# Kernel optimization log

Measured on AMD Instinct MI355X. Metric: run time of the kernel, lower is better.

The kernel has to match this reference:

```python
import jax, jax.numpy as jnp
import numpy as np

WINDOW_SIZES = (1, 2, 3)
COV_DIM = 128
MEM_DIM = 128
BATCH = 8192


def setup_inputs() -> dict:
    rng = np.random.default_rng(0)
    sizes = rng.integers(16, 64, size=BATCH)
    total = int(sizes.sum())  # ~327k tokens
    key = jax.random.key(0)
    ks = jax.random.split(key, 10)
    s = 0.05
    inp = {
        "x": jax.random.normal(ks[0], (total, COV_DIM), jnp.float32),
        "sizes": jnp.asarray(sizes, jnp.int32),
    }
    for i, w in enumerate(WINDOW_SIZES):
        inp[f"conv_w{i}"] = jax.random.normal(ks[1 + 2 * i], (MEM_DIM, COV_DIM, w), jnp.float32) * s
        inp[f"conv_b{i}"] = jax.random.normal(ks[2 + 2 * i], (MEM_DIM,), jnp.float32) * s
    inp["lin_w"] = jax.random.normal(ks[7], (MEM_DIM, len(WINDOW_SIZES) * MEM_DIM), jnp.float32) * s
    inp["lin_b"] = jax.random.normal(ks[8], (MEM_DIM,), jnp.float32) * s
    return inp


def _temporal_conv(x, w, b):
    # x: [T, C], w: [M, C, k] -> [T-k+1, M]  (valid 1D conv, as nn.Conv1d)
    y = jax.lax.conv_general_dilated(
        x.T[None],  # [1, C, T]
        w,
        window_strides=(1,),
        padding="VALID",
        dimension_numbers=("NCH", "OIH", "NCH"),
    )[0]  # [M, L]
    return y.T + b


def _dmax(h, sizes, window_size, batch):
    # Ragged per-segment max over dim 0 of the concatenated conv output.
    # Segment i covers rows [off_i, off_i + sizes[i] - window_size + 1) where
    # off_i is the exclusive cumsum of sizes (DMax advances start_idx by sizes[i]).
    L = h.shape[0]  # total - window_size + 1
    cum = jnp.cumsum(sizes)  # [B], inclusive
    p = jnp.arange(L)
    seg = jnp.searchsorted(cum, p, side="right")  # segment owning row p
    valid = p + (window_size - 1) < cum[seg]  # within sizes[i]-w+1 prefix
    seg = jnp.where(valid, seg, batch)  # dump invalid rows in a trash segment
    return jax.ops.segment_max(h, seg, num_segments=batch + 1)[:batch]


def reference(x, sizes, conv_w0, conv_b0, conv_w1, conv_b1, conv_w2, conv_b2, lin_w, lin_b):
    batch = sizes.shape[0]
    convs = ((conv_w0, conv_b0), (conv_w1, conv_b1), (conv_w2, conv_b2))
    pools = []
    for wsz, (cw, cb) in zip(WINDOW_SIZES, convs):
        h = jax.nn.relu(_temporal_conv(x, cw, cb))  # [T-w+1, M]
        pools.append(_dmax(h, sizes, wsz, batch))  # [B, M]
    concat = jnp.concatenate(pools, axis=1)  # [B, 3M]
    return jnp.tanh(concat @ lin_w.T + lin_b)  # [B, M]
```

## Files before the change

kernel.cpp:

```cpp
#include <hip/hip_runtime.h>
#include <hip/hip_bf16.h>

typedef __bf16 bf16x8 __attribute__((ext_vector_type(8)));
typedef __bf16 bf16x4 __attribute__((ext_vector_type(4)));
typedef float  f32x4  __attribute__((ext_vector_type(4)));

#define MFMA16(a, b, c) __builtin_amdgcn_mfma_f32_16x16x32_bf16((a), (b), (c), 0, 0, 0)

__global__ void k_prep(const int* __restrict__ sizes, int* __restrict__ offsets,
                       const float* __restrict__ w0, const float* __restrict__ w1,
                       const float* __restrict__ w2, const float* __restrict__ lw,
                       __bf16* __restrict__ Wpack,
                       __bf16* __restrict__ Lhi, __bf16* __restrict__ Llo) {
  const int bid = blockIdx.x, t = threadIdx.x;
  if (bid == 240) {
    __shared__ int part[256];
    const int base = t * 32;
    int v[32];
    int s = 0;
#pragma unroll
    for (int i = 0; i < 32; ++i) { v[i] = sizes[base + i]; s += v[i]; }
    part[t] = s;
    __syncthreads();
    for (int d = 1; d < 256; d <<= 1) {
      int add = (t >= d) ? part[t - d] : 0;
      __syncthreads();
      part[t] += add;
      __syncthreads();
    }
    int run = (t == 0) ? 0 : part[t - 1];
#pragma unroll
    for (int i = 0; i < 32; ++i) { offsets[base + i] = run; run += v[i]; }
  } else if (bid < 48) {
    const int nt = bid, sl = nt >> 3, f = nt & 7;
    const int kt = t >> 6, lane = t & 63;
    const float* src; int kw, jj;
    if      (sl == 0) { src = w0; kw = 1; jj = 0; }
    else if (sl == 1) { src = w1; kw = 2; jj = 0; }
    else if (sl == 2) { src = w1; kw = 2; jj = 1; }
    else if (sl == 3) { src = w2; kw = 3; jj = 0; }
    else if (sl == 4) { src = w2; kw = 3; jj = 1; }
    else              { src = w2; kw = 3; jj = 2; }
    const int feat  = f * 16 + (lane & 15);
    const int cbase = kt * 32 + ((lane >> 4) << 3);
    __bf16* dst = Wpack + ((((nt * 4 + kt) << 6) + lane) << 3);
#pragma unroll
    for (int j = 0; j < 8; ++j)
      dst[j] = (__bf16)src[(feat * 128 + cbase + j) * kw + jj];
  } else {
    const int idx = (bid - 48) * 256 + t;
    const int j = idx & 7, lane = (idx >> 3) & 63, rest = idx >> 9;
    const int kt = rest % 12, nt = rest / 12;
    const int o = nt * 16 + (lane & 15);
    const int q = kt * 32 + ((lane >> 4) << 3) + j;
    const float v = lw[o * 384 + q];
    const __bf16 hi = (__bf16)v;
    Lhi[idx] = hi;
    Llo[idx] = (__bf16)(v - (float)hi);
  }
}

__global__ __launch_bounds__(256, 3)
void k_conv(const float* __restrict__ x, const int* __restrict__ sizes,
            const int* __restrict__ offsets,
            const float* __restrict__ cb0, const float* __restrict__ cb1,
            const float* __restrict__ cb2,
            const bf16x8* __restrict__ Wpack,
            __bf16* __restrict__ Phi, __bf16* __restrict__ Plo) {
  __shared__ __bf16 xh[64 * 136];
  const int b = blockIdx.x;
  const int s = sizes[b];
  const long off = offsets[b];
  const int t = threadIdx.x;
  const int MT = (s + 15) >> 4;

  const int quads = s << 5;
  for (int qi = t; qi < quads; qi += 256) {
    const int e = qi << 2, r = e >> 7, c = e & 127;
    const float4 v = *(const float4*)(x + (off + r) * 128 + c);
    bf16x4 h; h[0] = (__bf16)v.x; h[1] = (__bf16)v.y;
              h[2] = (__bf16)v.z; h[3] = (__bf16)v.w;
    *(bf16x4*)&xh[r * 136 + c] = h;
  }
  const int padquads = ((MT << 4) - s) << 5;
  for (int qi = t; qi < padquads; qi += 256) {
    const int e = (qi << 2) + (s << 7), r = e >> 7, c = e & 127;
    *(bf16x4*)&xh[r * 136 + c] = bf16x4{(__bf16)0.f, (__bf16)0.f, (__bf16)0.f, (__bf16)0.f};
  }
  __syncthreads();

  const int wid = t >> 6, lane = t & 63;
  const int lo16 = lane & 15, g = lane >> 4;

#pragma unroll
  for (int fi = 0; fi < 2; ++fi) {
    const int ft = wid + (fi << 2);
    const int feat = ft * 16 + lo16;
    f32x4 acc[4][6];
#pragma unroll
    for (int mt = 0; mt < 4; ++mt)
#pragma unroll
      for (int sl = 0; sl < 6; ++sl)
        acc[mt][sl] = f32x4{0.f, 0.f, 0.f, 0.f};

#pragma unroll
    for (int kt = 0; kt < 4; ++kt) {
      bf16x8 bf[6];
#pragma unroll
      for (int sl = 0; sl < 6; ++sl)
        bf[sl] = Wpack[(((sl * 8 + ft) * 4 + kt) << 6) + lane];
#pragma unroll
      for (int mt = 0; mt < 4; ++mt) {
        if (mt < MT) {
          const bf16x8 a =
              *(const bf16x8*)&xh[(mt * 16 + lo16) * 136 + kt * 32 + (g << 3)];
#pragma unroll
          for (int sl = 0; sl < 6; ++sl)
            acc[mt][sl] = MFMA16(a, bf[sl], acc[mt][sl]);
        }
      }
    }

    float m1 = -1e30f, m2 = -1e30f, m3 = -1e30f;
#pragma unroll
    for (int mt = 0; mt < 4; ++mt) {
      if (mt >= MT) continue;
#pragma unroll
      for (int v = 0; v < 4; ++v) {
        float s2v;
        if (v < 3) {
          s2v = acc[mt][2][v + 1];
        } else {
          const float up = __shfl(acc[mt][2][0], lane + 16);
          const float dn = __shfl(acc[(mt < 3) ? mt + 1 : mt][2][0], lo16);
          s2v = (g < 3) ? up : dn;
        }
        float s4v;
        if (v < 3) {
          s4v = acc[mt][4][v + 1];
        } else {
          const float up = __shfl(acc[mt][4][0], lane + 16);
          const float dn = __shfl(acc[(mt < 3) ? mt + 1 : mt][4][0], lo16);
          s4v = (g < 3) ? up : dn;
        }
        float s5v;
        if (v < 2) {
          s5v = acc[mt][5][v + 2];
        } else {
          const float up = __shfl(acc[mt][5][v - 2], lane + 16);
          const float dn = __shfl(acc[(mt < 3) ? mt + 1 : mt][5][v - 2], lo16);
          s5v = (g < 3) ? up : dn;
        }
        const int lrow = mt * 16 + g * 4 + v;
        if (lrow < s)     m1 = fmaxf(m1, acc[mt][0][v]);
        if (lrow < s - 1) m2 = fmaxf(m2, acc[mt][1][v] + s2v);
        if (lrow < s - 2) m3 = fmaxf(m3, acc[mt][3][v] + s4v + s5v);
      }
    }
    m1 = fmaxf(m1, __shfl_xor(m1, 16)); m1 = fmaxf(m1, __shfl_xor(m1, 32));
    m2 = fmaxf(m2, __shfl_xor(m2, 16)); m2 = fmaxf(m2, __shfl_xor(m2, 32));
    m3 = fmaxf(m3, __shfl_xor(m3, 16)); m3 = fmaxf(m3, __shfl_xor(m3, 32));
    if (g == 0) {
      const float p1 = fmaxf(m1 + cb0[feat], 0.f);
      const float p2 = fmaxf(m2 + cb1[feat], 0.f);
      const float p3 = fmaxf(m3 + cb2[feat], 0.f);
      const __bf16 h1 = (__bf16)p1, h2 = (__bf16)p2, h3 = (__bf16)p3;
      Phi[(long)b * 384 + feat]       = h1;
      Plo[(long)b * 384 + feat]       = (__bf16)(p1 - (float)h1);
      Phi[(long)b * 384 + 128 + feat] = h2;
      Plo[(long)b * 384 + 128 + feat] = (__bf16)(p2 - (float)h2);
      Phi[(long)b * 384 + 256 + feat] = h3;
      Plo[(long)b * 384 + 256 + feat] = (__bf16)(p3 - (float)h3);
    }
  }
}

__global__ __launch_bounds__(256, 4)
void k_lin(const __bf16* __restrict__ Phi, const __bf16* __restrict__ Plo,
           const bf16x8* __restrict__ Lhi, const bf16x8* __restrict__ Llo,
           const float* __restrict__ lb, float* __restrict__ out) {
  __shared__ __bf16 ph[16 * 392];
  __shared__ __bf16 pl[16 * 392];
  const int blk = blockIdx.x, t = threadIdx.x;
  const long rbase = (long)blk * 16;
#pragma unroll
  for (int i = 0; i < 3; ++i) {
    const int ci = t + (i << 8);
    const int r = ci / 48, cc = ci % 48;
    *(int4*)&ph[r * 392 + (cc << 3)] = *(const int4*)&Phi[(rbase + r) * 384 + (cc << 3)];
    *(int4*)&pl[r * 392 + (cc << 3)] = *(const int4*)&Plo[(rbase + r) * 384 + (cc << 3)];
  }
  __syncthreads();
  const int wid = t >> 6, lane = t & 63;
  const int lo16 = lane & 15, g = lane >> 4;
#pragma unroll
  for (int ni = 0; ni < 2; ++ni) {
    const int nt = wid + (ni << 2);
    f32x4 acc = f32x4{0.f, 0.f, 0.f, 0.f};
#pragma unroll
    for (int kt = 0; kt < 12; ++kt) {
      const bf16x8 bh = Lhi[((nt * 12 + kt) << 6) + lane];
      const bf16x8 bl = Llo[((nt * 12 + kt) << 6) + lane];
      const int aoff = lo16 * 392 + kt * 32 + (g << 3);
      const bf16x8 ah = *(const bf16x8*)&ph[aoff];
      const bf16x8 al = *(const bf16x8*)&pl[aoff];
      acc = MFMA16(ah, bh, acc);
      acc = MFMA16(al, bh, acc);
      acc = MFMA16(ah, bl, acc);
    }
    const int o = nt * 16 + lo16;
    const float bias = lb[o];
#pragma unroll
    for (int v = 0; v < 4; ++v) {
      const int r = g * 4 + v;
      const float val = acc[v] + bias;
      out[(rbase + r) * 128 + o] = 1.f - 2.f / (__expf(2.f * val) + 1.f);
    }
  }
}

extern "C" void kernel_launch(void* const* d_in, const int* in_sizes, int n_in,
                              void* d_out, int out_size, void* d_ws, size_t ws_size,
                              hipStream_t stream) {
  const float* x   = (const float*)d_in[0];
  const int* sizes = (const int*)d_in[1];
  const float* w0  = (const float*)d_in[2];
  const float* cb0 = (const float*)d_in[3];
  const float* w1  = (const float*)d_in[4];
  const float* cb1 = (const float*)d_in[5];
  const float* w2  = (const float*)d_in[6];
  const float* cb2 = (const float*)d_in[7];
  const float* lw  = (const float*)d_in[8];
  const float* lb  = (const float*)d_in[9];

  char* ws = (char*)d_ws;
  size_t o = 0;
  int*    offsets = (int*)ws;                 o += 32768;
  __bf16* Wpack   = (__bf16*)(ws + o);        o += 196608;
  __bf16* Lhi     = (__bf16*)(ws + o);        o += 98304;
  __bf16* Llo     = (__bf16*)(ws + o);        o += 98304;
  __bf16* Phi     = (__bf16*)(ws + o);        o += 8192L * 384 * 2;
  __bf16* Plo     = (__bf16*)(ws + o);        o += 8192L * 384 * 2;

  k_prep<<<241, 256, 0, stream>>>(sizes, offsets, w0, w1, w2, lw, Wpack, Lhi, Llo);
  k_conv<<<8192, 256, 0, stream>>>(x, sizes, offsets, cb0, cb1, cb2,
                                   (const bf16x8*)Wpack, Phi, Plo);
  k_lin<<<512, 256, 0, stream>>>(Phi, Plo, (const bf16x8*)Lhi,
                                 (const bf16x8*)Llo, lb, (float*)d_out);
}
```

Baseline: 340.9 us.

## Process three segments per conv block to reuse weight fragments in registers

Each conv block now stages three segments into shared memory and loops over them, loading each weight fragment set once per block instead of once per segment. The six weight slices are split into two passes of three, which lowers accumulator register pressure while holding all four k-tiles of weights in registers. This cuts repeated global weight reads and the number of blocks, but triples LDS use per block (about 52KB), which limits occupancy. It also lengthens the serial work per block.

```diff
diff --git a/kernel.cpp b/kernel.cpp
--- a/kernel.cpp
+++ b/kernel.cpp
@@ -6,6 +6,8 @@
 typedef float  f32x4  __attribute__((ext_vector_type(4)));
 
 #define MFMA16(a, b, c) __builtin_amdgcn_mfma_f32_16x16x32_bf16((a), (b), (c), 0, 0, 0)
+
+#define SEGS_PER_BLOCK 3
 
 __global__ void k_prep(const int* __restrict__ sizes, int* __restrict__ offsets,
                        const float* __restrict__ w0, const float* __restrict__ w1,
@@ -67,110 +69,156 @@
             const float* __restrict__ cb2,
             const bf16x8* __restrict__ Wpack,
             __bf16* __restrict__ Phi, __bf16* __restrict__ Plo) {
-  __shared__ __bf16 xh[64 * 136];
-  const int b = blockIdx.x;
-  const int s = sizes[b];
-  const long off = offsets[b];
+  __shared__ __bf16 xh[SEGS_PER_BLOCK][64 * 136];
+  const int b0 = blockIdx.x * SEGS_PER_BLOCK;
+  const int segs = min(SEGS_PER_BLOCK, 8192 - b0);
   const int t = threadIdx.x;
-  const int MT = (s + 15) >> 4;
-
-  const int quads = s << 5;
-  for (int qi = t; qi < quads; qi += 256) {
-    const int e = qi << 2, r = e >> 7, c = e & 127;
-    const float4 v = *(const float4*)(x + (off + r) * 128 + c);
-    bf16x4 h; h[0] = (__bf16)v.x; h[1] = (__bf16)v.y;
-              h[2] = (__bf16)v.z; h[3] = (__bf16)v.w;
-    *(bf16x4*)&xh[r * 136 + c] = h;
-  }
-  const int padquads = ((MT << 4) - s) << 5;
-  for (int qi = t; qi < padquads; qi += 256) {
-    const int e = (qi << 2) + (s << 7), r = e >> 7, c = e & 127;
-    *(bf16x4*)&xh[r * 136 + c] = bf16x4{(__bf16)0.f, (__bf16)0.f, (__bf16)0.f, (__bf16)0.f};
+
+  int  sz[SEGS_PER_BLOCK];
+  long ofs[SEGS_PER_BLOCK];
+#pragma unroll
+  for (int g = 0; g < SEGS_PER_BLOCK; ++g) {
+    sz[g]  = (g < segs) ? sizes[b0 + g] : 0;
+    ofs[g] = (g < segs) ? (long)offsets[b0 + g] : 0;
+  }
+
+#pragma unroll
+  for (int g = 0; g < SEGS_PER_BLOCK; ++g) {
+    if (g >= segs) break;
+    const int s = sz[g];
+    const int MT = (s + 15) >> 4;
+    const long off = ofs[g];
+    __bf16* base = &xh[g][0];
+    const int quads = s << 5;
+    for (int qi = t; qi < quads; qi += 256) {
+      const int r = qi >> 5, c = (qi & 31) << 2;
+      const float4 v = *(const float4*)(x + (off + r) * 128 + c);
+      bf16x4 h; h[0] = (__bf16)v.x; h[1] = (__bf16)v.y;
+                h[2] = (__bf16)v.z; h[3] = (__bf16)v.w;
+      *(bf16x4*)&base[r * 136 + c] = h;
+    }
+    const int padquads = ((MT << 4) - s) << 5;
+    for (int qi = t; qi < padquads; qi += 256) {
+      const int e = (qi << 2) + (s << 7), r = e >> 7, c = e & 127;
+      *(bf16x4*)&base[r * 136 + c] =
+          bf16x4{(__bf16)0.f, (__bf16)0.f, (__bf16)0.f, (__bf16)0.f};
+    }
   }
   __syncthreads();
 
   const int wid = t >> 6, lane = t & 63;
-  const int lo16 = lane & 15, g = lane >> 4;
+  const int lo16 = lane & 15, g16 = lane >> 4;
 
 #pragma unroll
   for (int fi = 0; fi < 2; ++fi) {
     const int ft = wid + (fi << 2);
     const int feat = ft * 16 + lo16;
-    f32x4 acc[4][6];
-#pragma unroll
-    for (int mt = 0; mt < 4; ++mt)
-#pragma unroll
-      for (int sl = 0; sl < 6; ++sl)
-        acc[mt][sl] = f32x4{0.f, 0.f, 0.f, 0.f};
-
-#pragma unroll
-    for (int kt = 0; kt < 4; ++kt) {
-      bf16x8 bf[6];
-#pragma unroll
-      for (int sl = 0; sl < 6; ++sl)
-        bf[sl] = Wpack[(((sl * 8 + ft) * 4 + kt) << 6) + lane];
-#pragma unroll
-      for (int mt = 0; mt < 4; ++mt) {
-        if (mt < MT) {
-          const bf16x8 a =
-              *(const bf16x8*)&xh[(mt * 16 + lo16) * 136 + kt * 32 + (g << 3)];
-#pragma unroll
-          for (int sl = 0; sl < 6; ++sl)
-            acc[mt][sl] = MFMA16(a, bf[sl], acc[mt][sl]);
+#pragma unroll
+    for (int pass = 0; pass < 2; ++pass) {
+      bf16x8 bf[3][4];
+#pragma unroll
+      for (int sl = 0; sl < 3; ++sl)
+#pragma unroll
+        for (int kt = 0; kt < 4; ++kt)
+          bf[sl][kt] = Wpack[((((pass * 3 + sl) * 8 + ft) * 4 + kt) << 6) + lane];
+
+#pragma unroll
+      for (int g = 0; g < SEGS_PER_BLOCK; ++g) {
+        if (g >= segs) break;
+        const int s = sz[g];
+        const int MT = (s + 15) >> 4;
+        const __bf16* base = &xh[g][0];
+
+        f32x4 acc[4][3];
+#pragma unroll
+        for (int mt = 0; mt < 4; ++mt)
+#pragma unroll
+          for (int sl = 0; sl < 3; ++sl)
+            acc[mt][sl] = f32x4{0.f, 0.f, 0.f, 0.f};
+
+#pragma unroll
+        for (int kt = 0; kt < 4; ++kt) {
+#pragma unroll
+          for (int mt = 0; mt < 4; ++mt) {
+            if (mt < MT) {
+              const bf16x8 a =
+                  *(const bf16x8*)&base[(mt * 16 + lo16) * 136 + kt * 32 + (g16 << 3)];
+              acc[mt][0] = MFMA16(a, bf[0][kt], acc[mt][0]);
+              acc[mt][1] = MFMA16(a, bf[1][kt], acc[mt][1]);
+              acc[mt][2] = MFMA16(a, bf[2][kt], acc[mt][2]);
+            }
+          }
+        }
+
+        if (pass == 0) {
+          float m1 = -1e30f, m2 = -1e30f;
+#pragma unroll
+          for (int mt = 0; mt < 4; ++mt) {
+            if (mt >= MT) continue;
+#pragma unroll
+            for (int v = 0; v < 4; ++v) {
+              float s2v;
+              if (v < 3) {
+                s2v = acc[mt][2][v + 1];
+              } else {
+                const float up = __shfl(acc[mt][2][0], lane + 16);
+                const float dn = __shfl(acc[(mt < 3) ? mt + 1 : mt][2][0], lo16);
+                s2v = (g16 < 3) ? up : dn;
+              }
+              const int lrow = mt * 16 + g16 * 4 + v;
+              if (lrow < s)     m1 = fmaxf(m1, acc[mt][0][v]);
+              if (lrow < s - 1) m2 = fmaxf(m2, acc[mt][1][v] + s2v);
+            }
+          }
+          m1 = fmaxf(m1, __shfl_xor(m1, 16)); m1 = fmaxf(m1, __shfl_xor(m1, 32));
+          m2 = fmaxf(m2, __shfl_xor(m2, 16)); m2 = fmaxf(m2, __shfl_xor(m2, 32));
+          if (g16 == 0) {
+            const float p1 = fmaxf(m1 + cb0[feat], 0.f);
+            const float p2 = fmaxf(m2 + cb1[feat], 0.f);
+            const __bf16 h1 = (__bf16)p1, h2 = (__bf16)p2;
+            const long row = (long)(b0 + g) * 384;
+            Phi[row + feat]       = h1;
+            Plo[row + feat]       = (__bf16)(p1 - (float)h1);
+            Phi[row + 128 + feat] = h2;
+            Plo[row + 128 + feat] = (__bf16)(p2 - (float)h2);
+          }
+        } else {
+          float m3 = -1e30f;
+#pragma unroll
+          for (int mt = 0; mt < 4; ++mt) {
+            if (mt >= MT) continue;
+#pragma unroll
+            for (int v = 0; v < 4; ++v) {
+              float s4v;
+              if (v < 3) {
+                s4v = acc[mt][1][v + 1];
+              } else {
+                const float up = __shfl(acc[mt][1][0], lane + 16);
+                const float dn = __shfl(acc[(mt < 3) ? mt + 1 : mt][1][0], lo16);
+                s4v = (g16 < 3) ? up : dn;
+              }
+              float s5v;
+              if (v < 2) {
+                s5v = acc[mt][2][v + 2];
+              } else {
+                const float up = __shfl(acc[mt][2][v - 2], lane + 16);
+                const float dn = __shfl(acc[(mt < 3) ? mt + 1 : mt][2][v - 2], lo16);
+                s5v = (g16 < 3) ? up : dn;
+              }
+              const int lrow = mt * 16 + g16 * 4 + v;
+              if (lrow < s - 2) m3 = fmaxf(m3, acc[mt][0][v] + s4v + s5v);
+            }
+          }
+          m3 = fmaxf(m3, __shfl_xor(m3, 16)); m3 = fmaxf(m3, __shfl_xor(m3, 32));
+          if (g16 == 0) {
+            const float p3 = fmaxf(m3 + cb2[feat], 0.f);
+            const __bf16 h3 = (__bf16)p3;
+            const long row = (long)(b0 + g) * 384;
+            Phi[row + 256 + feat] = h3;
+            Plo[row + 256 + feat] = (__bf16)(p3 - (float)h3);
+          }
         }
       }
-    }
-
-    float m1 = -1e30f, m2 = -1e30f, m3 = -1e30f;
-#pragma unroll
-    for (int mt = 0; mt < 4; ++mt) {
-      if (mt >= MT) continue;
-#pragma unroll
-      for (int v = 0; v < 4; ++v) {
-        float s2v;
-        if (v < 3) {
-          s2v = acc[mt][2][v + 1];
-        } else {
-          const float up = __shfl(acc[mt][2][0], lane + 16);
-          const float dn = __shfl(acc[(mt < 3) ? mt + 1 : mt][2][0], lo16);
-          s2v = (g < 3) ? up : dn;
-        }
-        float s4v;
-        if (v < 3) {
-          s4v = acc[mt][4][v + 1];
-        } else {
-          const float up = __shfl(acc[mt][4][0], lane + 16);
-          const float dn = __shfl(acc[(mt < 3) ? mt + 1 : mt][4][0], lo16);
-          s4v = (g < 3) ? up : dn;
-        }
-        float s5v;
-        if (v < 2) {
-          s5v = acc[mt][5][v + 2];
-        } else {
-          const float up = __shfl(acc[mt][5][v - 2], lane + 16);
-          const float dn = __shfl(acc[(mt < 3) ? mt + 1 : mt][5][v - 2], lo16);
-          s5v = (g < 3) ? up : dn;
-        }
-        const int lrow = mt * 16 + g * 4 + v;
-        if (lrow < s)     m1 = fmaxf(m1, acc[mt][0][v]);
-        if (lrow < s - 1) m2 = fmaxf(m2, acc[mt][1][v] + s2v);
-        if (lrow < s - 2) m3 = fmaxf(m3, acc[mt][3][v] + s4v + s5v);
-      }
-    }
-    m1 = fmaxf(m1, __shfl_xor(m1, 16)); m1 = fmaxf(m1, __shfl_xor(m1, 32));
-    m2 = fmaxf(m2, __shfl_xor(m2, 16)); m2 = fmaxf(m2, __shfl_xor(m2, 32));
-    m3 = fmaxf(m3, __shfl_xor(m3, 16)); m3 = fmaxf(m3, __shfl_xor(m3, 32));
-    if (g == 0) {
-      const float p1 = fmaxf(m1 + cb0[feat], 0.f);
-      const float p2 = fmaxf(m2 + cb1[feat], 0.f);
-      const float p3 = fmaxf(m3 + cb2[feat], 0.f);
-      const __bf16 h1 = (__bf16)p1, h2 = (__bf16)p2, h3 = (__bf16)p3;
-      Phi[(long)b * 384 + feat]       = h1;
-      Plo[(long)b * 384 + feat]       = (__bf16)(p1 - (float)h1);
-      Phi[(long)b * 384 + 128 + feat] = h2;
-      Plo[(long)b * 384 + 128 + feat] = (__bf16)(p2 - (float)h2);
-      Phi[(long)b * 384 + 256 + feat] = h3;
-      Plo[(long)b * 384 + 256 + feat] = (__bf16)(p3 - (float)h3);
     }
   }
 }
@@ -242,9 +290,10 @@
   __bf16* Phi     = (__bf16*)(ws + o);        o += 8192L * 384 * 2;
   __bf16* Plo     = (__bf16*)(ws + o);        o += 8192L * 384 * 2;
 
+  const int nconv = (8192 + SEGS_PER_BLOCK - 1) / SEGS_PER_BLOCK;
   k_prep<<<241, 256, 0, stream>>>(sizes, offsets, w0, w1, w2, lw, Wpack, Lhi, Llo);
-  k_conv<<<8192, 256, 0, stream>>>(x, sizes, offsets, cb0, cb1, cb2,
-                                   (const bf16x8*)Wpack, Phi, Plo);
+  k_conv<<<nconv, 256, 0, stream>>>(x, sizes, offsets, cb0, cb1, cb2,
+                                    (const bf16x8*)Wpack, Phi, Plo);
   k_lin<<<512, 256, 0, stream>>>(Phi, Plo, (const bf16x8*)Lhi,
                                  (const bf16x8*)Llo, lb, (float*)d_out);
 }
```

After: 350.4 us. +2.8%, slower.

## Shift A rows in LDS to accumulate conv taps in MFMA, drop shuffles

Applied to the files above, without the earlier changes.

Instead of computing each conv tap into its own accumulator and combining them with cross-lane shuffles, the kernel now loads row-shifted A fragments (offset by one and two rows) from LDS. It accumulates all taps of each window into a single accumulator, cutting accumulators from six to three per tile. This lowers register pressure, so the launch bound rises to 4 blocks per CU, and the epilogue shuffles go away. The x staging loop is also restructured to issue all global loads before converting and storing, and two extra padding rows are zeroed. The cost is extra LDS reads per MFMA group and a slightly larger LDS buffer.

```diff
diff --git a/kernel.cpp b/kernel.cpp
--- a/kernel.cpp
+++ b/kernel.cpp
@@ -60,48 +60,63 @@
   }
 }
 
-__global__ __launch_bounds__(256, 3)
+__global__ __launch_bounds__(256, 4)
 void k_conv(const float* __restrict__ x, const int* __restrict__ sizes,
             const int* __restrict__ offsets,
             const float* __restrict__ cb0, const float* __restrict__ cb1,
             const float* __restrict__ cb2,
             const bf16x8* __restrict__ Wpack,
             __bf16* __restrict__ Phi, __bf16* __restrict__ Plo) {
-  __shared__ __bf16 xh[64 * 136];
+  __shared__ __bf16 xh[66 * 136];
   const int b = blockIdx.x;
   const int s = sizes[b];
   const long off = offsets[b];
   const int t = threadIdx.x;
   const int MT = (s + 15) >> 4;
 
-  const int quads = s << 5;
-  for (int qi = t; qi < quads; qi += 256) {
-    const int e = qi << 2, r = e >> 7, c = e & 127;
-    const float4 v = *(const float4*)(x + (off + r) * 128 + c);
-    bf16x4 h; h[0] = (__bf16)v.x; h[1] = (__bf16)v.y;
-              h[2] = (__bf16)v.z; h[3] = (__bf16)v.w;
-    *(bf16x4*)&xh[r * 136 + c] = h;
-  }
-  const int padquads = ((MT << 4) - s) << 5;
-  for (int qi = t; qi < padquads; qi += 256) {
-    const int e = (qi << 2) + (s << 7), r = e >> 7, c = e & 127;
-    *(bf16x4*)&xh[r * 136 + c] = bf16x4{(__bf16)0.f, (__bf16)0.f, (__bf16)0.f, (__bf16)0.f};
+  {
+    const int quads = s << 5;
+    float4 v[8];
+#pragma unroll
+    for (int i = 0; i < 8; ++i) {
+      const int qi = t + (i << 8);
+      if (qi < quads) {
+        const int r = qi >> 5, c = (qi & 31) << 2;
+        v[i] = *(const float4*)(x + (off + r) * 128 + c);
+      }
+    }
+#pragma unroll
+    for (int i = 0; i < 8; ++i) {
+      const int qi = t + (i << 8);
+      if (qi < quads) {
+        const int r = qi >> 5, c = (qi & 31) << 2;
+        bf16x4 h; h[0] = (__bf16)v[i].x; h[1] = (__bf16)v[i].y;
+                  h[2] = (__bf16)v[i].z; h[3] = (__bf16)v[i].w;
+        *(bf16x4*)&xh[r * 136 + c] = h;
+      }
+    }
+    const int zend = MT * 16 + 2;
+    const int c = (t & 31) << 2;
+    for (int r = s + (t >> 5); r < zend; r += 8)
+      *(bf16x4*)&xh[r * 136 + c] =
+          bf16x4{(__bf16)0.f, (__bf16)0.f, (__bf16)0.f, (__bf16)0.f};
   }
   __syncthreads();
 
   const int wid = t >> 6, lane = t & 63;
-  const int lo16 = lane & 15, g = lane >> 4;
+  const int lo16 = lane & 15, g16 = lane >> 4;
 
 #pragma unroll
   for (int fi = 0; fi < 2; ++fi) {
     const int ft = wid + (fi << 2);
     const int feat = ft * 16 + lo16;
-    f32x4 acc[4][6];
+
+    f32x4 acc[4][3];
 #pragma unroll
     for (int mt = 0; mt < 4; ++mt)
 #pragma unroll
-      for (int sl = 0; sl < 6; ++sl)
-        acc[mt][sl] = f32x4{0.f, 0.f, 0.f, 0.f};
+      for (int p = 0; p < 3; ++p)
+        acc[mt][p] = f32x4{0.f, 0.f, 0.f, 0.f};
 
 #pragma unroll
     for (int kt = 0; kt < 4; ++kt) {
@@ -112,11 +127,16 @@
 #pragma unroll
       for (int mt = 0; mt < 4; ++mt) {
         if (mt < MT) {
-          const bf16x8 a =
-              *(const bf16x8*)&xh[(mt * 16 + lo16) * 136 + kt * 32 + (g << 3)];
-#pragma unroll
-          for (int sl = 0; sl < 6; ++sl)
-            acc[mt][sl] = MFMA16(a, bf[sl], acc[mt][sl]);
+          const __bf16* ap = &xh[(mt * 16 + lo16) * 136 + kt * 32 + (g16 << 3)];
+          const bf16x8 A0 = *(const bf16x8*)ap;
+          const bf16x8 A1 = *(const bf16x8*)(ap + 136);
+          const bf16x8 A2 = *(const bf16x8*)(ap + 272);
+          acc[mt][0] = MFMA16(A0, bf[0], acc[mt][0]);
+          acc[mt][1] = MFMA16(A0, bf[1], acc[mt][1]);
+          acc[mt][1] = MFMA16(A1, bf[2], acc[mt][1]);
+          acc[mt][2] = MFMA16(A0, bf[3], acc[mt][2]);
+          acc[mt][2] = MFMA16(A1, bf[4], acc[mt][2]);
+          acc[mt][2] = MFMA16(A2, bf[5], acc[mt][2]);
         }
       }
     }
@@ -127,50 +147,27 @@
       if (mt >= MT) continue;
 #pragma unroll
       for (int v = 0; v < 4; ++v) {
-        float s2v;
-        if (v < 3) {
-          s2v = acc[mt][2][v + 1];
-        } else {
-          const float up = __shfl(acc[mt][2][0], lane + 16);
-          const float dn = __shfl(acc[(mt < 3) ? mt + 1 : mt][2][0], lo16);
-          s2v = (g < 3) ? up : dn;
-        }
-        float s4v;
-        if (v < 3) {
-          s4v = acc[mt][4][v + 1];
-        } else {
-          const float up = __shfl(acc[mt][4][0], lane + 16);
-          const float dn = __shfl(acc[(mt < 3) ? mt + 1 : mt][4][0], lo16);
-          s4v = (g < 3) ? up : dn;
-        }
-        float s5v;
-        if (v < 2) {
-          s5v = acc[mt][5][v + 2];
-        } else {
-          const float up = __shfl(acc[mt][5][v - 2], lane + 16);
-          const float dn = __shfl(acc[(mt < 3) ? mt + 1 : mt][5][v - 2], lo16);
-          s5v = (g < 3) ? up : dn;
-        }
-        const int lrow = mt * 16 + g * 4 + v;
+        const int lrow = mt * 16 + g16 * 4 + v;
         if (lrow < s)     m1 = fmaxf(m1, acc[mt][0][v]);
-        if (lrow < s - 1) m2 = fmaxf(m2, acc[mt][1][v] + s2v);
-        if (lrow < s - 2) m3 = fmaxf(m3, acc[mt][3][v] + s4v + s5v);
+        if (lrow < s - 1) m2 = fmaxf(m2, acc[mt][1][v]);
+        if (lrow < s - 2) m3 = fmaxf(m3, acc[mt][2][v]);
       }
     }
     m1 = fmaxf(m1, __shfl_xor(m1, 16)); m1 = fmaxf(m1, __shfl_xor(m1, 32));
     m2 = fmaxf(m2, __shfl_xor(m2, 16)); m2 = fmaxf(m2, __shfl_xor(m2, 32));
     m3 = fmaxf(m3, __shfl_xor(m3, 16)); m3 = fmaxf(m3, __shfl_xor(m3, 32));
-    if (g == 0) {
+    if (g16 == 0) {
       const float p1 = fmaxf(m1 + cb0[feat], 0.f);
       const float p2 = fmaxf(m2 + cb1[feat], 0.f);
       const float p3 = fmaxf(m3 + cb2[feat], 0.f);
       const __bf16 h1 = (__bf16)p1, h2 = (__bf16)p2, h3 = (__bf16)p3;
-      Phi[(long)b * 384 + feat]       = h1;
-      Plo[(long)b * 384 + feat]       = (__bf16)(p1 - (float)h1);
-      Phi[(long)b * 384 + 128 + feat] = h2;
-      Plo[(long)b * 384 + 128 + feat] = (__bf16)(p2 - (float)h2);
-      Phi[(long)b * 384 + 256 + feat] = h3;
-      Plo[(long)b * 384 + 256 + feat] = (__bf16)(p3 - (float)h3);
+      const long row = (long)b * 384;
+      Phi[row + feat]       = h1;
+      Plo[row + feat]       = (__bf16)(p1 - (float)h1);
+      Phi[row + 128 + feat] = h2;
+      Plo[row + 128 + feat] = (__bf16)(p2 - (float)h2);
+      Phi[row + 256 + feat] = h3;
+      Plo[row + 256 + feat] = (__bf16)(p3 - (float)h3);
     }
   }
 }
```

Result: faster. 326.4 us (-4.2%).
